# Optimization experiments

Measured on AMD Instinct MI355X. Metric: run time of the kernel, lower is better.

The kernel has to match this reference:

```python
import jax, jax.numpy as jnp
import numpy as np

D_MODEL = 512
NHEAD = 8
MAX_REL = 256  # max_relative_position


def _linear(x, w, b):
    # torch nn.Linear: y = x @ W^T + b, W: [out, in]
    return jnp.einsum('...i,oi->...o', x, w) + b


def setup_inputs() -> dict:
    key = jax.random.key(0)
    ks = jax.random.split(key, 16)
    B, S, D = 32, 512, D_MODEL
    s = 0.02
    inp = {
        'query': jax.random.normal(ks[0], (B, S, D), jnp.float32),
        'key':   jax.random.normal(ks[1], (B, S, D), jnp.float32),
        'value': jax.random.normal(ks[2], (B, S, D), jnp.float32),
        # local attention projections (torch Linear weights [out,in])
        'wq': jax.random.normal(ks[3], (D, D), jnp.float32) * s,
        'bq': jnp.zeros((D,), jnp.float32),
        'wk': jax.random.normal(ks[4], (D, D), jnp.float32) * s,
        'bk': jnp.zeros((D,), jnp.float32),
        'wv': jax.random.normal(ks[5], (D, D), jnp.float32) * s,
        'bv': jnp.zeros((D,), jnp.float32),
        'wo': jax.random.normal(ks[6], (D, D), jnp.float32) * s,
        'bo': jnp.zeros((D,), jnp.float32),
        # relative-position key embedding table [2*MAX_REL+1, head_dim]
        'rel_k': jax.random.normal(ks[7], (2 * MAX_REL + 1, D // NHEAD), jnp.float32) * s,
        # global nn.MultiheadAttention (nhead//2 heads): packed in_proj + out_proj
        'g_in_w': jax.random.normal(ks[8], (3 * D, D), jnp.float32) * s,
        'g_in_b': jnp.zeros((3 * D,), jnp.float32),
        'g_out_w': jax.random.normal(ks[9], (D, D), jnp.float32) * s,
        'g_out_b': jnp.zeros((D,), jnp.float32),
    }
    return inp


def reference(query, key, value, wq, bq, wk, bk, wv, bv, wo, bo, rel_k,
              g_in_w, g_in_b, g_out_w, g_out_b):
    B, S, D = query.shape
    H, hd = NHEAD, D // NHEAD

    # --- local attention with relative-position bias ---
    q = _linear(query, wq, bq).reshape(B, S, H, hd).transpose(0, 2, 1, 3)  # [B,H,S,hd]
    k = _linear(key,   wk, bk).reshape(B, S, H, hd).transpose(0, 2, 1, 3)
    v = _linear(value, wv, bv).reshape(B, S, H, hd).transpose(0, 2, 1, 3)

    scores = jnp.einsum('bhqd,bhkd->bhqk', q, k) / jnp.sqrt(jnp.float32(hd))

    # relative positions: distance[i,j] = j - i, clamped, shifted to [0, 2*MAX_REL]
    idx = jnp.arange(S)
    rel_ids = jnp.clip(idx[None, :] - idx[:, None], -MAX_REL, MAX_REL) + MAX_REL  # [S,S]
    rel_pos_k = rel_k[rel_ids]  # [S, S, hd]
    scores = scores + jnp.einsum('bhld,lrd->bhlr', q, rel_pos_k)

    attn = jax.nn.softmax(scores, axis=-1)
    local = jnp.einsum('bhqk,bhkd->bhqd', attn, v)
    local = local.transpose(0, 2, 1, 3).reshape(B, S, D)

    # --- global MHA with H//2 heads ---
    Hg = H // 2
    hdg = D // Hg
    qg = _linear(query, g_in_w[:D], g_in_b[:D]).reshape(B, S, Hg, hdg).transpose(0, 2, 1, 3)
    kg = _linear(key,   g_in_w[D:2 * D], g_in_b[D:2 * D]).reshape(B, S, Hg, hdg).transpose(0, 2, 1, 3)
    vg = _linear(value, g_in_w[2 * D:], g_in_b[2 * D:]).reshape(B, S, Hg, hdg).transpose(0, 2, 1, 3)
    gs = jnp.einsum('bhqd,bhkd->bhqk', qg, kg) / jnp.sqrt(jnp.float32(hdg))
    ga = jax.nn.softmax(gs, axis=-1)
    g = jnp.einsum('bhqk,bhkd->bhqd', ga, vg).transpose(0, 2, 1, 3).reshape(B, S, D)
    g = _linear(g, g_out_w, g_out_b)

    combined = 0.7 * local + 0.3 * g
    return _linear(combined, wo, bo)
```

## Files before the change

kernel.cpp:

```cpp
#include <hip/hip_runtime.h>

typedef __attribute__((ext_vector_type(8))) short bh8;
typedef __attribute__((ext_vector_type(4))) float f4;

#define DEVI static __device__ __forceinline__

DEVI unsigned short f2b(float f) {
  union { float f; unsigned u; } v; v.f = f;
  unsigned r = v.u + 0x7fffu + ((v.u >> 16) & 1u);
  return (unsigned short)(r >> 16);
}
DEVI float b2f(unsigned short h) {
  union { unsigned u; float f; } v; v.u = ((unsigned)h) << 16;
  return v.f;
}
DEVI f4 mfma16(bh8 a, bh8 b, f4 c) {
  return __builtin_amdgcn_mfma_f32_16x16x32_bf16(a, b, c, 0, 0, 0);
}
DEVI void gload_lds16(const unsigned short* g, unsigned short* l) {
  __builtin_amdgcn_global_load_lds(
      (const __attribute__((address_space(1))) void*)(g),
      (__attribute__((address_space(3))) void*)(l), 16, 0, 0);
}

__global__ __launch_bounds__(256) void prep_x_kern(
    const float* __restrict__ q, const float* __restrict__ k, const float* __restrict__ v,
    unsigned short* __restrict__ xq, unsigned short* __restrict__ xk, unsigned short* __restrict__ xv) {
  long i = ((long)blockIdx.x * 256 + threadIdx.x) * 4;
  if (i >= 8388608L) return;
  float4 a = *(const float4*)(q + i);
  float4 b = *(const float4*)(k + i);
  float4 c = *(const float4*)(v + i);
  union { unsigned short s[4]; uint2 u; } pa, pb, pc;
  pa.s[0] = f2b(a.x); pa.s[1] = f2b(a.y); pa.s[2] = f2b(a.z); pa.s[3] = f2b(a.w);
  pb.s[0] = f2b(b.x); pb.s[1] = f2b(b.y); pb.s[2] = f2b(b.z); pb.s[3] = f2b(b.w);
  pc.s[0] = f2b(c.x); pc.s[1] = f2b(c.y); pc.s[2] = f2b(c.z); pc.s[3] = f2b(c.w);
  *(uint2*)(xq + i) = pa.u;
  *(uint2*)(xk + i) = pb.u;
  *(uint2*)(xv + i) = pc.u;
}

__global__ __launch_bounds__(256) void prep_w_kern(
    const float* __restrict__ wq, const float* __restrict__ wk, const float* __restrict__ wv,
    const float* __restrict__ g_in_w, const float* __restrict__ g_out_w,
    const float* __restrict__ wo, const float* __restrict__ rel_k,
    const float* __restrict__ bgo, const float* __restrict__ bo,
    unsigned short* __restrict__ Wq, unsigned short* __restrict__ Wk, unsigned short* __restrict__ Wv,
    unsigned short* __restrict__ Wo_, unsigned short* __restrict__ WgoT,
    unsigned short* __restrict__ Bfin, unsigned short* __restrict__ Rk,
    float* __restrict__ bias2) {
  if (blockIdx.x >= 2337) {
    int o = (blockIdx.x - 2337) * 256 + threadIdx.x;
    if (o < 512) {
      const float* r = wo + (long)o * 512;
      float s = 0.f;
#pragma unroll 4
      for (int m = 0; m < 512; m += 4) {
        float4 a = *(const float4*)(r + m);
        float4 b = *(const float4*)(bgo + m);
        s += a.x * b.x + a.y * b.y + a.z * b.z + a.w * b.w;
      }
      bias2[o] = bo[o] + 0.3f * s;
    }
    return;
  }
  long i = ((long)blockIdx.x * 256 + threadIdx.x) * 4;
  if (i >= 2392128L) return;
  if (i >= 2097152L && i < 2359296L) {
    long off = i - 2097152L;
    int ii = (int)(off >> 9), p = (int)(off & 511);
    union { unsigned short s[4]; uint2 u; } w;
#pragma unroll
    for (int tt = 0; tt < 4; tt++) w.s[tt] = f2b(g_out_w[(p + tt) * 512 + ii]);
    *(uint2*)(WgoT + off) = w.u;
    return;
  }
  const float* src; unsigned short* dst; long off; float sc = 1.0f;
  if (i < 524288L)        { dst = Wq;  off = i; src = (i < 262144L) ? wq + i : g_in_w + (i - 262144L); }
  else if (i < 1048576L)  { long j = i - 524288L;  dst = Wk;  off = j; src = (j < 262144L) ? wk + j : g_in_w + j; }
  else if (i < 1572864L)  { long j = i - 1048576L; dst = Wv;  off = j; src = (j < 262144L) ? wv + j : g_in_w + 262144L + j; }
  else if (i < 1835008L)  { long j = i - 1572864L; dst = Wo_; off = j; src = wo + j; }
  else if (i < 2097152L)  { long j = i - 1835008L; int col = (int)(j >> 9), k = (int)(j & 511);
                            dst = Bfin; off = (long)col * 1024 + k; src = wo + j; sc = 0.7f; }
  else                    { long j = i - 2359296L; dst = Rk;  off = j; src = rel_k + j; }
  float4 f = *(const float4*)src;
  union { unsigned short s[4]; uint2 u; } p;
  p.s[0] = f2b(f.x * sc); p.s[1] = f2b(f.y * sc); p.s[2] = f2b(f.z * sc); p.s[3] = f2b(f.w * sc);
  *(uint2*)(dst + off) = p.u;
}

__global__ __launch_bounds__(256) void gemm3_kern(
    const unsigned short* __restrict__ Xq, const unsigned short* __restrict__ Xk,
    const unsigned short* __restrict__ Xv,
    const unsigned short* __restrict__ Wq, const unsigned short* __restrict__ Wk,
    const unsigned short* __restrict__ Wv,
    const float* __restrict__ bq, const float* __restrict__ bk, const float* __restrict__ bv,
    const float* __restrict__ g_in_b,
    unsigned short* __restrict__ Yq, unsigned short* __restrict__ Yk_,
    unsigned short* __restrict__ Yvt_l, unsigned short* __restrict__ Yvt_g,
    const unsigned short* __restrict__ Wo_, const unsigned short* __restrict__ WgoT,
    unsigned short* __restrict__ Bfin) {
  __shared__ unsigned short lsA[128 * 32];
  __shared__ unsigned short lsB[128 * 32];
  const int t = threadIdx.x;
  const int lane = t & 63, w = t >> 6;
  const int l15 = lane & 15, g = lane >> 4, g4 = g * 4;
  const int gs8 = (g ^ ((l15 >> 1) & 3)) * 8;
  const int n = blockIdx.x;

  const unsigned short *Ap, *Bp;
  const float *b0 = nullptr, *b1 = nullptr;
  int seg, rb, cb;
  if (n < 3072) {
    seg = n >> 10;
    int m = n & 1023;
    int x = m >> 3, c = m & 7;
    rb = (c * 16 + (x & 15)) * 128;
    cb = (x >> 4) * 128;
    Ap = (seg == 0) ? Xq : (seg == 1) ? Xk : Xv;
    Bp = (seg == 0) ? Wq : (seg == 1) ? Wk : Wv;
    b0 = (seg == 0) ? bq : (seg == 1) ? bk : bv;
    b1 = g_in_b + seg * 512;
  } else {
    seg = 3;
    int m2 = n - 3072;
    rb = (m2 & 3) * 128; cb = (m2 >> 2) * 128;
    Ap = Wo_; Bp = WgoT;
  }

  const int wr = (w >> 1) * 64, wc = (w & 1) * 64;
  const int r0 = t >> 2, r1 = 64 + (t >> 2);
  const int k0i = ((t & 3) ^ ((t >> 3) & 3)) * 8;

  const unsigned short* pa0 = Ap + (long)(rb + r0) * 512 + k0i;
  const unsigned short* pa1 = Ap + (long)(rb + r1) * 512 + k0i;
  const unsigned short* pb0 = Bp + (long)(cb + r0) * 512 + k0i;
  const unsigned short* pb1 = Bp + (long)(cb + r1) * 512 + k0i;
  unsigned short* dA0 = lsA + w * 512;
  unsigned short* dA1 = lsA + 2048 + w * 512;
  unsigned short* dB0 = lsB + w * 512;
  unsigned short* dB1 = lsB + 2048 + w * 512;

  f4 acc[4][4] = {};
  for (int k0 = 0; k0 < 512; k0 += 32) {
    __syncthreads();
    gload_lds16(pa0 + k0, dA0);
    gload_lds16(pa1 + k0, dA1);
    gload_lds16(pb0 + k0, dB0);
    gload_lds16(pb1 + k0, dB1);
    __syncthreads();
    bh8 af[4], bf[4];
#pragma unroll
    for (int m = 0; m < 4; m++) af[m] = *(const bh8*)(lsA + (wr + m * 16 + l15) * 32 + gs8);
#pragma unroll
    for (int nn = 0; nn < 4; nn++) bf[nn] = *(const bh8*)(lsB + (wc + nn * 16 + l15) * 32 + gs8);
    __builtin_amdgcn_s_setprio(1);
#pragma unroll
    for (int m = 0; m < 4; m++)
#pragma unroll
      for (int nn = 0; nn < 4; nn++)
        acc[m][nn] = mfma16(af[m], bf[nn], acc[m][nn]);
    __builtin_amdgcn_s_setprio(0);
  }

  if (seg == 3) {
#pragma unroll
// ... 28 lines not shown
        if (col < 512) {
          int hh = col >> 6, d = col & 63;
          *(uint2*)(Yvt_l + (((long)(bb * 8 + hh) * 64 + d) << 9) + s) = make_uint2(lo, hi);
        } else {
          int c2 = col - 512, hg = c2 >> 7, dg = c2 & 127;
          *(uint2*)(Yvt_g + (((long)(bb * 4 + hg) * 128 + dg) << 9) + s) = make_uint2(lo, hi);
        }
      }
    return;
  }
  unsigned short* Yo = (seg == 0) ? Yq : Yk_;
#pragma unroll
  for (int m = 0; m < 4; m++)
#pragma unroll
    for (int nn = 0; nn < 4; nn++)
#pragma unroll
      for (int j = 0; j < 4; j++) {
        int row = rb + wr + m * 16 + g4 + j;
        int col = cb + wc + nn * 16 + l15;
        float v = acc[m][nn][j] + ((col < 512) ? b0[col] : b1[col - 512]);
        Yo[(long)row * 1024 + col] = f2b(v);
      }
}

__global__ __launch_bounds__(256) void gemm_fin_kern(
    const unsigned short* __restrict__ A, const unsigned short* __restrict__ Bw,
    const float* __restrict__ bias0, float* __restrict__ outf) {
  __shared__ unsigned short lsA[128 * 32];
  __shared__ unsigned short lsB[128 * 32];
  const int t = threadIdx.x;
  const int lane = t & 63, w = t >> 6;
  const int l15 = lane & 15, g = lane >> 4, g4 = g * 4;
  const int gs8 = (g ^ ((l15 >> 1) & 3)) * 8;
  int n = blockIdx.x;
  int x = n >> 3, c = n & 7;
  const int rb = (c * 16 + (x & 15)) * 128;
  const int cb = (x >> 4) * 128;
  const int wr = (w >> 1) * 64, wc = (w & 1) * 64;
  const int r0 = t >> 2, r1 = 64 + (t >> 2);
  const int k0i = ((t & 3) ^ ((t >> 3) & 3)) * 8;

  const unsigned short* pa0 = A + (long)(rb + r0) * 1024 + k0i;
  const unsigned short* pa1 = A + (long)(rb + r1) * 1024 + k0i;
  const unsigned short* pb0 = Bw + (long)(cb + r0) * 1024 + k0i;
  const unsigned short* pb1 = Bw + (long)(cb + r1) * 1024 + k0i;
  unsigned short* dA0 = lsA + w * 512;
  unsigned short* dA1 = lsA + 2048 + w * 512;
  unsigned short* dB0 = lsB + w * 512;
  unsigned short* dB1 = lsB + 2048 + w * 512;

  f4 acc[4][4] = {};
  for (int k0 = 0; k0 < 1024; k0 += 32) {
    __syncthreads();
    gload_lds16(pa0 + k0, dA0);
    gload_lds16(pa1 + k0, dA1);
    gload_lds16(pb0 + k0, dB0);
    gload_lds16(pb1 + k0, dB1);
    __syncthreads();
    bh8 af[4], bf[4];
#pragma unroll
    for (int m = 0; m < 4; m++) af[m] = *(const bh8*)(lsA + (wr + m * 16 + l15) * 32 + gs8);
#pragma unroll
    for (int nn = 0; nn < 4; nn++) bf[nn] = *(const bh8*)(lsB + (wc + nn * 16 + l15) * 32 + gs8);
    __builtin_amdgcn_s_setprio(1);
#pragma unroll
    for (int m = 0; m < 4; m++)
#pragma unroll
      for (int nn = 0; nn < 4; nn++)
        acc[m][nn] = mfma16(af[m], bf[nn], acc[m][nn]);
    __builtin_amdgcn_s_setprio(0);
  }
#pragma unroll
  for (int m = 0; m < 4; m++)
#pragma unroll
    for (int nn = 0; nn < 4; nn++)
#pragma unroll
      for (int j = 0; j < 4; j++) {
        int row = rb + wr + m * 16 + g4 + j;
        int col = cb + wc + nn * 16 + l15;
        outf[(long)row * 512 + col] = acc[m][nn][j] + bias0[col];
      }
}

__global__ __launch_bounds__(512, 4) void attn_local_kern(
    const unsigned short* __restrict__ Yq, const unsigned short* __restrict__ Yk,
    const unsigned short* __restrict__ Yvt, const unsigned short* __restrict__ relk,
    unsigned short* __restrict__ outC) {
  __shared__ unsigned short kv[2][8192];
  __shared__ unsigned short buf[32 * 524];
  __shared__ float redbuf[8][32];

  const int t = threadIdx.x, lane = t & 63, w = t >> 6;
  const int l15 = lane & 15, g = lane >> 4, g8 = g * 8;
  int n = blockIdx.x;
  int bid = (n & 7) * 512 + (n >> 3);
  const int qt = bid & 15;
  const int h = (bid >> 4) & 7;
  const int b = bid >> 7;
  const int qb = qt * 32;
  const long base = ((long)(b * 512)) * 1024 + h * 64;
  const long vbase = ((long)(b * 8 + h)) * 64 * 512;

#define STAGE_K(ROFF, BUF) { \
    const int c_ = t & 7; \
    _Pragma("unroll") \
    for (int it = 0; it < 2; it++) { \
      int rr = it * 64 + (t >> 3); \
      gload_lds16(Yk + base + (long)((ROFF) + rr) * 1024 + ((c_ ^ (rr & 7)) * 8), \
                  kv[BUF] + it * 4096 + w * 512); \
    } }
#define STAGE_V(COFF, BUF) { \
    const int c_ = t & 15; \
    _Pragma("unroll") \
    for (int it = 0; it < 2; it++) { \
      int dd_ = it * 32 + (t >> 4); \
      gload_lds16(Yvt + vbase + (long)dd_ * 512 + (COFF) + ((c_ ^ (dd_ & 15)) * 8), \
                  kv[BUF] + it * 4096 + w * 512); \
    } }
#define QK(CH) { \
    int rl = w * 16 + l15; \
    const unsigned short* kb_ = kv[(CH) & 1]; \
    bh8 k0 = *(const bh8*)(kb_ + rl * 64 + ((g ^ (rl & 7)) * 8)); \
    bh8 k1 = *(const bh8*)(kb_ + rl * 64 + (((g + 4) ^ (rl & 7)) * 8)); \
    _Pragma("unroll") \
    for (int mm = 0; mm < 2; mm++) { \
      f4 a = {}; \
      a = mfma16(qf[mm][0], k0, a); \
      a = mfma16(qf[mm][1], k1, a); \
      sc[mm][CH] = a; \
    } }
#define GATHER(CH) { \
    _Pragma("unroll") \
    for (int mm = 0; mm < 2; mm++) \
    _Pragma("unroll") \
    for (int j = 0; j < 4; j++) { \
      int lr = mm * 16 + g * 4 + j; \
      int rowb = lr * 524; \
      int idx = rowb + 256 - (qb + lr) + (CH) * 128 + w * 16 + l15; \
      idx = idx < rowb ? rowb : idx; \
      idx = idx > rowb + 512 ? rowb + 512 : idx; \
      float p = exp2f(fmaf(sc[mm][CH][j], 0.18033688011112042f, b2f(buf[idx]))); \
      sc[mm][CH][j] = p; \
      rs[mm][j] += p; \
    } }

  STAGE_K(0, 0);

  bh8 qf[2][2];
#pragma unroll
  for (int mm = 0; mm < 2; mm++) {
    const unsigned short* qp = Yq + base + (long)(qb + mm * 16 + l15) * 1024 + g8;
    qf[mm][0] = *(const bh8*)(qp);
    qf[mm][1] = *(const bh8*)(qp + 32);
  }

  for (int tt = w; tt < 33; tt += 8) {
    int ri = tt * 16 + l15; if (ri > 512) ri = 512;
    const unsigned short* rp = relk + ri * 64 + g8;
    bh8 rf0 = *(const bh8*)(rp), rf1 = *(const bh8*)(rp + 32);
    int col = tt * 16 + l15;
#pragma unroll
    for (int mm = 0; mm < 2; mm++) {
      f4 a = {};
      a = mfma16(qf[mm][0], rf0, a);
      a = mfma16(qf[mm][1], rf1, a);
      if (col < 524) {
#pragma unroll
        for (int j = 0; j < 4; j++)
          buf[(mm * 16 + g * 4 + j) * 524 + col] = f2b(a[j] * 1.4426950408889634f);
      }
    }
  }
  __syncthreads();

  f4 sc[2][4];
  float rs[2][4] = {};

#pragma unroll
  for (int c = 0; c < 4; c++) {
    if (c < 3) { STAGE_K((c + 1) * 128, (c + 1) & 1); }
    else       { STAGE_V(0, 0); }
    __builtin_amdgcn_s_setprio(1);
    QK(c);
    __builtin_amdgcn_s_setprio(0);
    GATHER(c);
    __syncthreads();
  }

#pragma unroll
  for (int mm = 0; mm < 2; mm++)
#pragma unroll
    for (int j = 0; j < 4; j++) {
      int lr = mm * 16 + g * 4 + j;
      float s = rs[mm][j];
      for (int d = 1; d < 16; d <<= 1) s += __shfl_xor(s, d, 64);
      if (l15 == 0) redbuf[w][lr] = s;
    }
#pragma unroll
  for (int mm = 0; mm < 2; mm++)
#pragma unroll
    for (int ch = 0; ch < 4; ch++) {
      int col = ch * 128 + w * 16 + l15;
#pragma unroll
      for (int j = 0; j < 4; j++)
        buf[(mm * 16 + g * 4 + j) * 524 + col] = f2b(sc[mm][ch][j]);
    }
  __syncthreads();

  const int mmw = w >> 2, dt = w & 3;
  const int dd = dt * 16 + l15;
  float rinvj[4];
#pragma unroll
  for (int j = 0; j < 4; j++) {
    int lr = mmw * 16 + g * 4 + j;
    float s = 0.f;
#pragma unroll
    for (int ww = 0; ww < 8; ww++) s += redbuf[ww][lr];
    rinvj[j] = __builtin_amdgcn_rcpf(s);
  }

  f4 accO = {};
#pragma unroll
  for (int d = 0; d < 4; d++) {
    if (d < 3) { STAGE_V((d + 1) * 128, (d + 1) & 1); }
    const unsigned short* vb_ = kv[d & 1];
    __builtin_amdgcn_s_setprio(1);
#pragma unroll
    for (int ks2 = 0; ks2 < 4; ks2++) {
      union { uint2 u[2]; bh8 v; } pa;
      const unsigned short* pp = buf + (mmw * 16 + l15) * 524 + (d * 4 + ks2) * 32 + g8;
      pa.u[0] = *(const uint2*)(pp);
      pa.u[1] = *(const uint2*)(pp + 4);
      bh8 vv = *(const bh8*)(vb_ + dd * 128 + (((ks2 * 4 + g) ^ (dd & 15)) * 8));
      accO = mfma16(pa.v, vv, accO);
    }
    __builtin_amdgcn_s_setprio(0);
    if (d < 3) __syncthreads();
  }
#pragma unroll
  for (int j = 0; j < 4; j++) {
    int row = qb + mmw * 16 + g * 4 + j;
    outC[((long)(b * 512 + row)) * 1024 + h * 64 + dt * 16 + l15] = f2b(accO[j] * rinvj[j]);
  }
#undef STAGE_K
#undef STAGE_V
#undef QK
#undef GATHER
}

__global__ __launch_bounds__(512) void attn_glob_kern(
    const unsigned short* __restrict__ Yq, const unsigned short* __restrict__ Yk,
    const unsigned short* __restrict__ Yvt, unsigned short* __restrict__ outC) {
  __shared__ unsigned short buf[32 * 520];
  __shared__ float redbuf[8][32];

  const int t = threadIdx.x, lane = t & 63, w = t >> 6;
  const int l15 = lane & 15, g = lane >> 4, g8 = g * 8;
  int n = blockIdx.x;
  int bid = (n & 7) * 256 + (n >> 3);
  const int qt = bid & 15;
  const int hg = (bid >> 4) & 3;
  const int b = bid >> 6;
  const int qb = qt * 32;
  const long base = ((long)(b * 512)) * 1024 + 512 + hg * 128;

  bh8 qf[2][4];
#pragma unroll
  for (int mm = 0; mm < 2; mm++) {
    const unsigned short* qp = Yq + base + (long)(qb + mm * 16 + l15) * 1024 + g8;
#pragma unroll
    for (int ks = 0; ks < 4; ks++) qf[mm][ks] = *(const bh8*)(qp + ks * 32);
  }

  f4 sc[2][4];
  __builtin_amdgcn_s_setprio(1);
#pragma unroll
  for (int ct = 0; ct < 4; ct++) {
    int r = w * 64 + ct * 16 + l15;
    const unsigned short* kp = Yk + base + (long)r * 1024 + g8;
    bh8 kf[4];
#pragma unroll
    for (int ks = 0; ks < 4; ks++) kf[ks] = *(const bh8*)(kp + ks * 32);
#pragma unroll
    for (int mm = 0; mm < 2; mm++) {
      f4 a = {};
#pragma unroll
      for (int ks = 0; ks < 4; ks++) a = mfma16(qf[mm][ks], kf[ks], a);
      sc[mm][ct] = a;
    }
  }
  __builtin_amdgcn_s_setprio(0);

#pragma unroll
  for (int mm = 0; mm < 2; mm++) {
#pragma unroll
    for (int j = 0; j < 4; j++) {
      int lr = mm * 16 + g * 4 + j;
      float s = 0.f;
#pragma unroll
      for (int ct = 0; ct < 4; ct++) {
        float p = exp2f(sc[mm][ct][j] * 0.12751745334f);
        sc[mm][ct][j] = p;
        s += p;
      }
      for (int d = 1; d < 16; d <<= 1) s += __shfl_xor(s, d, 64);
      if (l15 == 0) redbuf[w][lr] = s;
    }
  }
#pragma unroll
  for (int mm = 0; mm < 2; mm++)
#pragma unroll
    for (int ct = 0; ct < 4; ct++) {
      int col = w * 64 + ct * 16 + l15;
#pragma unroll
      for (int j = 0; j < 4; j++)
        buf[(mm * 16 + g * 4 + j) * 520 + col] = f2b(sc[mm][ct][j]);
    }
  __syncthreads();

  float rinv[2][4];
#pragma unroll
  for (int mm = 0; mm < 2; mm++)
#pragma unroll
    for (int j = 0; j < 4; j++) {
      int lr = mm * 16 + g * 4 + j;
      float s = 0.f;
#pragma unroll
      for (int ww = 0; ww < 8; ww++) s += redbuf[ww][lr];
      rinv[mm][j] = __builtin_amdgcn_rcpf(s);
    }

  f4 accO[2] = {};
  const unsigned short* vr = Yvt + ((long)(b * 4 + hg) * 128 + w * 16 + l15) * 512;
  __builtin_amdgcn_s_setprio(1);
#pragma unroll
  for (int ks = 0; ks < 16; ks++) {
    bh8 vb = *(const bh8*)(vr + ks * 32 + g8);
#pragma unroll
    for (int mm = 0; mm < 2; mm++) {
      union { uint2 u[2]; bh8 v; } pa;
      const unsigned short* pp = buf + (mm * 16 + l15) * 520 + ks * 32 + g8;
      pa.u[0] = *(const uint2*)(pp);
      pa.u[1] = *(const uint2*)(pp + 4);
      accO[mm] = mfma16(pa.v, vb, accO[mm]);
    }
  }
  __builtin_amdgcn_s_setprio(0);
#pragma unroll
  for (int mm = 0; mm < 2; mm++)
#pragma unroll
    for (int j = 0; j < 4; j++) {
      int row = qb + mm * 16 + g * 4 + j;
      outC[((long)(b * 512 + row)) * 1024 + 512 + hg * 128 + w * 16 + l15] = f2b(accO[mm][j] * rinv[mm][j]);
    }
}

extern "C" void kernel_launch(void* const* d_in, const int* in_sizes, int n_in,
                              void* d_out, int out_size, void* d_ws, size_t ws_size,
                              hipStream_t stream) {
  const float* query = (const float*)d_in[0];
  const float* key   = (const float*)d_in[1];
  const float* value = (const float*)d_in[2];
  const float* wq = (const float*)d_in[3];   const float* bq = (const float*)d_in[4];
  const float* wk = (const float*)d_in[5];   const float* bk = (const float*)d_in[6];
  const float* wv = (const float*)d_in[7];   const float* bv = (const float*)d_in[8];
  const float* wo = (const float*)d_in[9];   const float* bo = (const float*)d_in[10];
  const float* rel_k = (const float*)d_in[11];
  const float* g_in_w = (const float*)d_in[12];  const float* g_in_b = (const float*)d_in[13];
  const float* g_out_w = (const float*)d_in[14]; const float* g_out_b = (const float*)d_in[15];

  unsigned short* p = (unsigned short*)d_ws;
  unsigned short* Xq = p;            p += 8388608;
  unsigned short* Xk = p;            p += 8388608;
  unsigned short* Xv = p;            p += 8388608;
  unsigned short* Yq = p;            p += 16777216;
  unsigned short* Yk = p;            p += 16777216;
  unsigned short* Yvt_l = p;         p += 8388608;
  unsigned short* Yvt_g = p;         p += 8388608;
  unsigned short* Wq = p;            p += 524288;
  unsigned short* Wk = p;            p += 524288;
  unsigned short* Wv = p;            p += 524288;
  unsigned short* Wo_ = p;           p += 262144;
  unsigned short* WgoT = p;          p += 262144;
  unsigned short* Bfin = p;          p += 524288;
  unsigned short* Rk = p;            p += 32832;
  float* bias2 = (float*)p;          p += 1024;
  unsigned short* CAT = Xq;

  prep_x_kern<<<8192, 256, 0, stream>>>(query, key, value, Xq, Xk, Xv);
  prep_w_kern<<<2339, 256, 0, stream>>>(wq, wk, wv, g_in_w, g_out_w, wo, rel_k,
                                        g_out_b, bo,
                                        Wq, Wk, Wv, Wo_, WgoT, Bfin, Rk, bias2);

  gemm3_kern<<<3088, 256, 0, stream>>>(Xq, Xk, Xv, Wq, Wk, Wv, bq, bk, bv, g_in_b,
                                       Yq, Yk, Yvt_l, Yvt_g, Wo_, WgoT, Bfin);

  attn_local_kern<<<4096, 512, 0, stream>>>(Yq, Yk, Yvt_l, Rk, CAT);
  attn_glob_kern<<<2048, 512, 0, stream>>>(Yq, Yk, Yvt_g, CAT);

  gemm_fin_kern<<<512, 256, 0, stream>>>(CAT, Bfin, bias2, (float*)d_out);
}
```

Baseline: 342.4 us.

## Merge prep kernels and interleave local/global attention into one launch

Combines the activation and weight conversion kernels into a single launch. It also fuses the local and global attention kernels into one grid, interleaving two local blocks per global block so both kinds run concurrently. The intent is to remove launch overhead and the tail and idle gaps between dependent-free kernels. In exchange, the global path now shares the local path's register bounds and its larger shared-memory allocation, which may reduce its occupancy.

After: 341.2 us. Within noise of the previous version (-0.3%).

```diff
diff --git a/kernel.cpp b/kernel.cpp
--- a/kernel.cpp
+++ b/kernel.cpp
@@ -23,34 +23,34 @@
       (__attribute__((address_space(3))) void*)(l), 16, 0, 0);
 }
 
-__global__ __launch_bounds__(256) void prep_x_kern(
+__global__ __launch_bounds__(256) void prep_all_kern(
     const float* __restrict__ q, const float* __restrict__ k, const float* __restrict__ v,
-    unsigned short* __restrict__ xq, unsigned short* __restrict__ xk, unsigned short* __restrict__ xv) {
-  long i = ((long)blockIdx.x * 256 + threadIdx.x) * 4;
-  if (i >= 8388608L) return;
-  float4 a = *(const float4*)(q + i);
-  float4 b = *(const float4*)(k + i);
-  float4 c = *(const float4*)(v + i);
-  union { unsigned short s[4]; uint2 u; } pa, pb, pc;
-  pa.s[0] = f2b(a.x); pa.s[1] = f2b(a.y); pa.s[2] = f2b(a.z); pa.s[3] = f2b(a.w);
-  pb.s[0] = f2b(b.x); pb.s[1] = f2b(b.y); pb.s[2] = f2b(b.z); pb.s[3] = f2b(b.w);
-  pc.s[0] = f2b(c.x); pc.s[1] = f2b(c.y); pc.s[2] = f2b(c.z); pc.s[3] = f2b(c.w);
-  *(uint2*)(xq + i) = pa.u;
-  *(uint2*)(xk + i) = pb.u;
-  *(uint2*)(xv + i) = pc.u;
-}
-
-__global__ __launch_bounds__(256) void prep_w_kern(
     const float* __restrict__ wq, const float* __restrict__ wk, const float* __restrict__ wv,
     const float* __restrict__ g_in_w, const float* __restrict__ g_out_w,
     const float* __restrict__ wo, const float* __restrict__ rel_k,
     const float* __restrict__ bgo, const float* __restrict__ bo,
+    unsigned short* __restrict__ xq, unsigned short* __restrict__ xk, unsigned short* __restrict__ xv,
     unsigned short* __restrict__ Wq, unsigned short* __restrict__ Wk, unsigned short* __restrict__ Wv,
     unsigned short* __restrict__ Wo_, unsigned short* __restrict__ WgoT,
     unsigned short* __restrict__ Bfin, unsigned short* __restrict__ Rk,
     float* __restrict__ bias2) {
-  if (blockIdx.x >= 2337) {
-    int o = (blockIdx.x - 2337) * 256 + threadIdx.x;
+  if (blockIdx.x < 8192) {
+    long i = ((long)blockIdx.x * 256 + threadIdx.x) * 4;
+    float4 a = *(const float4*)(q + i);
+    float4 b = *(const float4*)(k + i);
+    float4 c = *(const float4*)(v + i);
+    union { unsigned short s[4]; uint2 u; } pa, pb, pc;
+    pa.s[0] = f2b(a.x); pa.s[1] = f2b(a.y); pa.s[2] = f2b(a.z); pa.s[3] = f2b(a.w);
+    pb.s[0] = f2b(b.x); pb.s[1] = f2b(b.y); pb.s[2] = f2b(b.z); pb.s[3] = f2b(b.w);
+    pc.s[0] = f2b(c.x); pc.s[1] = f2b(c.y); pc.s[2] = f2b(c.z); pc.s[3] = f2b(c.w);
+    *(uint2*)(xq + i) = pa.u;
+    *(uint2*)(xk + i) = pb.u;
+    *(uint2*)(xv + i) = pc.u;
+    return;
+  }
+  int bw = blockIdx.x - 8192;
+  if (bw >= 2337) {
+    int o = (bw - 2337) * 256 + threadIdx.x;
     if (o < 512) {
       const float* r = wo + (long)o * 512;
       float s = 0.f;
@@ -64,7 +64,7 @@
     }
     return;
   }
-  long i = ((long)blockIdx.x * 256 + threadIdx.x) * 4;
+  long i = ((long)bw * 256 + threadIdx.x) * 4;
   if (i >= 2392128L) return;
   if (i >= 2097152L && i < 2359296L) {
     long off = i - 2097152L;
@@ -80,8 +80,8 @@
   else if (i < 1048576L)  { long j = i - 524288L;  dst = Wk;  off = j; src = (j < 262144L) ? wk + j : g_in_w + j; }
   else if (i < 1572864L)  { long j = i - 1048576L; dst = Wv;  off = j; src = (j < 262144L) ? wv + j : g_in_w + 262144L + j; }
   else if (i < 1835008L)  { long j = i - 1572864L; dst = Wo_; off = j; src = wo + j; }
-  else if (i < 2097152L)  { long j = i - 1835008L; int col = (int)(j >> 9), k = (int)(j & 511);
-                            dst = Bfin; off = (long)col * 1024 + k; src = wo + j; sc = 0.7f; }
+  else if (i < 2097152L)  { long j = i - 1835008L; int col = (int)(j >> 9), kk = (int)(j & 511);
+                            dst = Bfin; off = (long)col * 1024 + kk; src = wo + j; sc = 0.7f; }
   else                    { long j = i - 2359296L; dst = Rk;  off = j; src = rel_k + j; }
   float4 f = *(const float4*)src;
   union { unsigned short s[4]; uint2 u; } p;
@@ -276,24 +276,28 @@
       }
 }
 
-__global__ __launch_bounds__(512, 4) void attn_local_kern(
+__global__ __launch_bounds__(512, 4) void attn_kern(
     const unsigned short* __restrict__ Yq, const unsigned short* __restrict__ Yk,
-    const unsigned short* __restrict__ Yvt, const unsigned short* __restrict__ relk,
-    unsigned short* __restrict__ outC) {
+    const unsigned short* __restrict__ Yvt_l, const unsigned short* __restrict__ Yvt_g,
+    const unsigned short* __restrict__ relk, unsigned short* __restrict__ outC) {
   __shared__ unsigned short kv[2][8192];
   __shared__ unsigned short buf[32 * 524];
   __shared__ float redbuf[8][32];
 
   const int t = threadIdx.x, lane = t & 63, w = t >> 6;
   const int l15 = lane & 15, g = lane >> 4, g8 = g * 8;
-  int n = blockIdx.x;
-  int bid = (n & 7) * 512 + (n >> 3);
-  const int qt = bid & 15;
-  const int h = (bid >> 4) & 7;
-  const int b = bid >> 7;
-  const int qb = qt * 32;
-  const long base = ((long)(b * 512)) * 1024 + h * 64;
-  const long vbase = ((long)(b * 8 + h)) * 64 * 512;
+  const int n = blockIdx.x;
+  const int grp = n / 3, r3 = n - grp * 3;
+
+  if (r3 < 2) {
+    int ln = grp * 2 + r3;
+    int bid = (ln & 7) * 512 + (ln >> 3);
+    const int qt = bid & 15;
+    const int h = (bid >> 4) & 7;
+    const int b = bid >> 7;
+    const int qb = qt * 32;
+    const long base = ((long)(b * 512)) * 1024 + h * 64;
+    const long vbase = ((long)(b * 8 + h)) * 64 * 512;
 
 #define STAGE_K(ROFF, BUF) { \
     const int c_ = t & 7; \
@@ -308,7 +312,7 @@
     _Pragma("unroll") \
     for (int it = 0; it < 2; it++) { \
       int dd_ = it * 32 + (t >> 4); \
-      gload_lds16(Yvt + vbase + (long)dd_ * 512 + (COFF) + ((c_ ^ (dd_ & 15)) * 8), \
+      gload_lds16(Yvt_l + vbase + (long)dd_ * 512 + (COFF) + ((c_ ^ (dd_ & 15)) * 8), \
                   kv[BUF] + it * 4096 + w * 512); \
     } }
 #define QK(CH) { \
@@ -338,215 +342,207 @@
       rs[mm][j] += p; \
     } }
 
-  STAGE_K(0, 0);
-
-  bh8 qf[2][2];
-#pragma unroll
-  for (int mm = 0; mm < 2; mm++) {
-    const unsigned short* qp = Yq + base + (long)(qb + mm * 16 + l15) * 1024 + g8;
-    qf[mm][0] = *(const bh8*)(qp);
-    qf[mm][1] = *(const bh8*)(qp + 32);
-  }
-
-  for (int tt = w; tt < 33; tt += 8) {
-    int ri = tt * 16 + l15; if (ri > 512) ri = 512;
-    const unsigned short* rp = relk + ri * 64 + g8;
-    bh8 rf0 = *(const bh8*)(rp), rf1 = *(const bh8*)(rp + 32);
-    int col = tt * 16 + l15;
+    STAGE_K(0, 0);
+
+    bh8 qf[2][2];
 #pragma unroll
     for (int mm = 0; mm < 2; mm++) {
-      f4 a = {};
-      a = mfma16(qf[mm][0], rf0, a);
-      a = mfma16(qf[mm][1], rf1, a);
-      if (col < 524) {
+      const unsigned short* qp = Yq + base + (long)(qb + mm * 16 + l15) * 1024 + g8;
+      qf[mm][0] = *(const bh8*)(qp);
+      qf[mm][1] = *(const bh8*)(qp + 32);
+    }
+
+    for (int tt = w; tt < 33; tt += 8) {
+      int ri = tt * 16 + l15; if (ri > 512) ri = 512;
+      const unsigned short* rp = relk + ri * 64 + g8;
+      bh8 rf0 = *(const bh8*)(rp), rf1 = *(const bh8*)(rp + 32);
+      int col = tt * 16 + l15;
+#pragma unroll
+      for (int mm = 0; mm < 2; mm++) {
+        f4 a = {};
+        a = mfma16(qf[mm][0], rf0, a);
+        a = mfma16(qf[mm][1], rf1, a);
+        if (col < 524) {
+#pragma unroll
+          for (int j = 0; j < 4; j++)
+            buf[(mm * 16 + g * 4 + j) * 524 + col] = f2b(a[j] * 1.4426950408889634f);
+        }
+      }
+    }
+    __syncthreads();
+
+    f4 sc[2][4];
+    float rs[2][4] = {};
+
+#pragma unroll
+    for (int c = 0; c < 4; c++) {
+      if (c < 3) { STAGE_K((c + 1) * 128, (c + 1) & 1); }
+      else       { STAGE_V(0, 0); }
+      __builtin_amdgcn_s_setprio(1);
+      QK(c);
+      __builtin_amdgcn_s_setprio(0);
+      GATHER(c);
+      __syncthreads();
+    }
+
+#pragma unroll
+    for (int mm = 0; mm < 2; mm++)
+#pragma unroll
+      for (int j = 0; j < 4; j++) {
+        int lr = mm * 16 + g * 4 + j;
+        float s = rs[mm][j];
+        for (int d = 1; d < 16; d <<= 1) s += __shfl_xor(s, d, 64);
+        if (l15 == 0) redbuf[w][lr] = s;
+      }
+#pragma unroll
+    for (int mm = 0; mm < 2; mm++)
+#pragma unroll
+      for (int ch = 0; ch < 4; ch++) {
+        int col = ch * 128 + w * 16 + l15;
 #pragma unroll
         for (int j = 0; j < 4; j++)
-          buf[(mm * 16 + g * 4 + j) * 524 + col] = f2b(a[j] * 1.4426950408889634f);
-      }
-    }
-  }
-  __syncthreads();
-
-  f4 sc[2][4];
-  float rs[2][4] = {};
-
-#pragma unroll
-  for (int c = 0; c < 4; c++) {
-    if (c < 3) { STAGE_K((c + 1) * 128, (c + 1) & 1); }
-    else       { STAGE_V(0, 0); }
-    __builtin_amdgcn_s_setprio(1);
-    QK(c);
-    __builtin_amdgcn_s_setprio(0);
-    GATHER(c);
-    __syncthreads();
-  }
-
-#pragma unroll
-  for (int mm = 0; mm < 2; mm++)
+          buf[(mm * 16 + g * 4 + j) * 524 + col] = f2b(sc[mm][ch][j]);
+      }
+    __syncthreads();
+
+    const int mmw = w >> 2, dt = w & 3;
+    const int dd = dt * 16 + l15;
+    float rinvj[4];
 #pragma unroll
     for (int j = 0; j < 4; j++) {
-      int lr = mm * 16 + g * 4 + j;
-      float s = rs[mm][j];
-      for (int d = 1; d < 16; d <<= 1) s += __shfl_xor(s, d, 64);
-      if (l15 == 0) redbuf[w][lr] = s;
-    }
-#pragma unroll
-  for (int mm = 0; mm < 2; mm++)
-#pragma unroll
-    for (int ch = 0; ch < 4; ch++) {
-      int col = ch * 128 + w * 16 + l15;
-#pragma unroll
-      for (int j = 0; j < 4; j++)
-        buf[(mm * 16 + g * 4 + j) * 524 + col] = f2b(sc[mm][ch][j]);
-    }
-  __syncthreads();
-
-  const int mmw = w >> 2, dt = w & 3;
-  const int dd = dt * 16 + l15;
-  float rinvj[4];
-#pragma unroll
-  for (int j = 0; j < 4; j++) {
-    int lr = mmw * 16 + g * 4 + j;
-    float s = 0.f;
-#pragma unroll
-    for (int ww = 0; ww < 8; ww++) s += redbuf[ww][lr];
-    rinvj[j] = __builtin_amdgcn_rcpf(s);
-  }
-
-  f4 accO = {};
-#pragma unroll
-  for (int d = 0; d < 4; d++) {
-    if (d < 3) { STAGE_V((d + 1) * 128, (d + 1) & 1); }
-    const unsigned short* vb_ = kv[d & 1];
-    __builtin_amdgcn_s_setprio(1);
-#pragma unroll
-    for (int ks2 = 0; ks2 < 4; ks2++) {
-      union { uint2 u[2]; bh8 v; } pa;
-      const unsigned short* pp = buf + (mmw * 16 + l15) * 524 + (d * 4 + ks2) * 32 + g8;
-      pa.u[0] = *(const uint2*)(pp);
-      pa.u[1] = *(const uint2*)(pp + 4);
-      bh8 vv = *(const bh8*)(vb_ + dd * 128 + (((ks2 * 4 + g) ^ (dd & 15)) * 8));
-      accO = mfma16(pa.v, vv, accO);
-    }
-    __builtin_amdgcn_s_setprio(0);
-    if (d < 3) __syncthreads();
-  }
-#pragma unroll
-  for (int j = 0; j < 4; j++) {
-    int row = qb + mmw * 16 + g * 4 + j;
-    outC[((long)(b * 512 + row)) * 1024 + h * 64 + dt * 16 + l15] = f2b(accO[j] * rinvj[j]);
-  }
+      int lr = mmw * 16 + g * 4 + j;
+      float s = 0.f;
+#pragma unroll
+      for (int ww = 0; ww < 8; ww++) s += redbuf[ww][lr];
+      rinvj[j] = __builtin_amdgcn_rcpf(s);
+    }
+
+    f4 accO = {};
+#pragma unroll
+    for (int d = 0; d < 4; d++) {
+      if (d < 3) { STAGE_V((d + 1) * 128, (d + 1) & 1); }
+      const unsigned short* vb_ = kv[d & 1];
+      __builtin_amdgcn_s_setprio(1);
+#pragma unroll
+      for (int ks2 = 0; ks2 < 4; ks2++) {
+        union { uint2 u[2]; bh8 v; } pa;
+        const unsigned short* pp = buf + (mmw * 16 + l15) * 524 + (d * 4 + ks2) * 32 + g8;
+        pa.u[0] = *(const uint2*)(pp);
+        pa.u[1] = *(const uint2*)(pp + 4);
+        bh8 vv = *(const bh8*)(vb_ + dd * 128 + (((ks2 * 4 + g) ^ (dd & 15)) * 8));
+        accO = mfma16(pa.v, vv, accO);
+      }
+      __builtin_amdgcn_s_setprio(0);
+      if (d < 3) __syncthreads();
+    }
+#pragma unroll
+    for (int j = 0; j < 4; j++) {
+      int row = qb + mmw * 16 + g * 4 + j;
+      outC[((long)(b * 512 + row)) * 1024 + h * 64 + dt * 16 + l15] = f2b(accO[j] * rinvj[j]);
+    }
 #undef STAGE_K
 #undef STAGE_V
 #undef QK
 #undef GATHER
-}
-
-__global__ __launch_bounds__(512) void attn_glob_kern(
-    const unsigned short* __restrict__ Yq, const unsigned short* __restrict__ Yk,
-    const unsigned short* __restrict__ Yvt, unsigned short* __restrict__ outC) {
-  __shared__ unsigned short buf[32 * 520];
-  __shared__ float redbuf[8][32];
-
-  const int t = threadIdx.x, lane = t & 63, w = t >> 6;
-  const int l15 = lane & 15, g = lane >> 4, g8 = g * 8;
-  int n = blockIdx.x;
-  int bid = (n & 7) * 256 + (n >> 3);
-  const int qt = bid & 15;
-  const int hg = (bid >> 4) & 3;
-  const int b = bid >> 6;
-  const int qb = qt * 32;
-  const long base = ((long)(b * 512)) * 1024 + 512 + hg * 128;
-
-  bh8 qf[2][4];
-#pragma unroll
-  for (int mm = 0; mm < 2; mm++) {
-    const unsigned short* qp = Yq + base + (long)(qb + mm * 16 + l15) * 1024 + g8;
-#pragma unroll
-    for (int ks = 0; ks < 4; ks++) qf[mm][ks] = *(const bh8*)(qp + ks * 32);
-  }
-
-  f4 sc[2][4];
-  __builtin_amdgcn_s_setprio(1);
-#pragma unroll
-  for (int ct = 0; ct < 4; ct++) {
-    int r = w * 64 + ct * 16 + l15;
-    const unsigned short* kp = Yk + base + (long)r * 1024 + g8;
-    bh8 kf[4];
-#pragma unroll
-    for (int ks = 0; ks < 4; ks++) kf[ks] = *(const bh8*)(kp + ks * 32);
+  } else {
+    int gn = grp;
+    int bid = (gn & 7) * 256 + (gn >> 3);
+    const int qt = bid & 15;
+    const int hg = (bid >> 4) & 3;
+    const int b = bid >> 6;
+    const int qb = qt * 32;
+    const long base = ((long)(b * 512)) * 1024 + 512 + hg * 128;
+
+    bh8 qf[2][4];
 #pragma unroll
     for (int mm = 0; mm < 2; mm++) {
-      f4 a = {};
-#pragma unroll
-      for (int ks = 0; ks < 4; ks++) a = mfma16(qf[mm][ks], kf[ks], a);
-      sc[mm][ct] = a;
-    }
-  }
-  __builtin_amdgcn_s_setprio(0);
-
-#pragma unroll
-  for (int mm = 0; mm < 2; mm++) {
-#pragma unroll
-    for (int j = 0; j < 4; j++) {
-      int lr = mm * 16 + g * 4 + j;
-      float s = 0.f;
+      const unsigned short* qp = Yq + base + (long)(qb + mm * 16 + l15) * 1024 + g8;
+#pragma unroll
+      for (int ks = 0; ks < 4; ks++) qf[mm][ks] = *(const bh8*)(qp + ks * 32);
+    }
+
+    f4 sc[2][4];
+    __builtin_amdgcn_s_setprio(1);
+#pragma unroll
+    for (int ct = 0; ct < 4; ct++) {
+      int r = w * 64 + ct * 16 + l15;
+      const unsigned short* kp = Yk + base + (long)r * 1024 + g8;
+      bh8 kf[4];
+#pragma unroll
+      for (int ks = 0; ks < 4; ks++) kf[ks] = *(const bh8*)(kp + ks * 32);
+#pragma unroll
+      for (int mm = 0; mm < 2; mm++) {
+        f4 a = {};
+#pragma unroll
+        for (int ks = 0; ks < 4; ks++) a = mfma16(qf[mm][ks], kf[ks], a);
+        sc[mm][ct] = a;
+      }
+    }
+    __builtin_amdgcn_s_setprio(0);
+
+#pragma unroll
+    for (int mm = 0; mm < 2; mm++) {
+#pragma unroll
+      for (int j = 0; j < 4; j++) {
+        int lr = mm * 16 + g * 4 + j;
+        float s = 0.f;
+#pragma unroll
+        for (int ct = 0; ct < 4; ct++) {
+          float p = exp2f(sc[mm][ct][j] * 0.12751745334f);
+          sc[mm][ct][j] = p;
+          s += p;
+        }
+        for (int d = 1; d < 16; d <<= 1) s += __shfl_xor(s, d, 64);
+        if (l15 == 0) redbuf[w][lr] = s;
+      }
+    }
+#pragma unroll
+    for (int mm = 0; mm < 2; mm++)
 #pragma unroll
       for (int ct = 0; ct < 4; ct++) {
-        float p = exp2f(sc[mm][ct][j] * 0.12751745334f);
-        sc[mm][ct][j] = p;
-        s += p;
-      }
-      for (int d = 1; d < 16; d <<= 1) s += __shfl_xor(s, d, 64);
-      if (l15 == 0) redbuf[w][lr] = s;
-    }
-  }
-#pragma unroll
-  for (int mm = 0; mm < 2; mm++)
-#pragma unroll
-    for (int ct = 0; ct < 4; ct++) {
-      int col = w * 64 + ct * 16 + l15;
-#pragma unroll
-      for (int j = 0; j < 4; j++)
-        buf[(mm * 16 + g * 4 + j) * 520 + col] = f2b(sc[mm][ct][j]);
-    }
-  __syncthreads();
-
-  float rinv[2][4];
-#pragma unroll
-  for (int mm = 0; mm < 2; mm++)
-#pragma unroll
-    for (int j = 0; j < 4; j++) {
-      int lr = mm * 16 + g * 4 + j;
-      float s = 0.f;
-#pragma unroll
-      for (int ww = 0; ww < 8; ww++) s += redbuf[ww][lr];
-      rinv[mm][j] = __builtin_amdgcn_rcpf(s);
-    }
-
-  f4 accO[2] = {};
-  const unsigned short* vr = Yvt + ((long)(b * 4 + hg) * 128 + w * 16 + l15) * 512;
-  __builtin_amdgcn_s_setprio(1);
-#pragma unroll
-  for (int ks = 0; ks < 16; ks++) {
-    bh8 vb = *(const bh8*)(vr + ks * 32 + g8);
-#pragma unroll
-    for (int mm = 0; mm < 2; mm++) {
-      union { uint2 u[2]; bh8 v; } pa;
-      const unsigned short* pp = buf + (mm * 16 + l15) * 520 + ks * 32 + g8;
-      pa.u[0] = *(const uint2*)(pp);
-      pa.u[1] = *(const uint2*)(pp + 4);
-      accO[mm] = mfma16(pa.v, vb, accO[mm]);
-    }
-  }
-  __builtin_amdgcn_s_setprio(0);
-#pragma unroll
-  for (int mm = 0; mm < 2; mm++)
-#pragma unroll
-    for (int j = 0; j < 4; j++) {
-      int row = qb + mm * 16 + g * 4 + j;
-      outC[((long)(b * 512 + row)) * 1024 + 512 + hg * 128 + w * 16 + l15] = f2b(accO[mm][j] * rinv[mm][j]);
-    }
+        int col = w * 64 + ct * 16 + l15;
+#pragma unroll
+        for (int j = 0; j < 4; j++)
+          buf[(mm * 16 + g * 4 + j) * 524 + col] = f2b(sc[mm][ct][j]);
+      }
+    __syncthreads();
+
+    float rinv[2][4];
+#pragma unroll
+    for (int mm = 0; mm < 2; mm++)
+#pragma unroll
+      for (int j = 0; j < 4; j++) {
+        int lr = mm * 16 + g * 4 + j;
+        float s = 0.f;
+#pragma unroll
+        for (int ww = 0; ww < 8; ww++) s += redbuf[ww][lr];
+        rinv[mm][j] = __builtin_amdgcn_rcpf(s);
+      }
+
+    f4 accO[2] = {};
+    const unsigned short* vr = Yvt_g + ((long)(b * 4 + hg) * 128 + w * 16 + l15) * 512;
+    __builtin_amdgcn_s_setprio(1);
+#pragma unroll
+    for (int ks = 0; ks < 16; ks++) {
+      bh8 vb = *(const bh8*)(vr + ks * 32 + g8);
+#pragma unroll
+      for (int mm = 0; mm < 2; mm++) {
+        union { uint2 u[2]; bh8 v; } pa;
+        const unsigned short* pp = buf + (mm * 16 + l15) * 524 + ks * 32 + g8;
+        pa.u[0] = *(const uint2*)(pp);
+        pa.u[1] = *(const uint2*)(pp + 4);
+        accO[mm] = mfma16(pa.v, vb, accO[mm]);
+      }
+    }
+    __builtin_amdgcn_s_setprio(0);
+#pragma unroll
+    for (int mm = 0; mm < 2; mm++)
+#pragma unroll
+      for (int j = 0; j < 4; j++) {
+        int row = qb + mm * 16 + g * 4 + j;
+        outC[((long)(b * 512 + row)) * 1024 + 512 + hg * 128 + w * 16 + l15] = f2b(accO[mm][j] * rinv[mm][j]);
+      }
+  }
 }
 
 extern "C" void kernel_launch(void* const* d_in, const int* in_sizes, int n_in,
@@ -581,16 +577,15 @@
   float* bias2 = (float*)p;          p += 1024;
   unsigned short* CAT = Xq;
 
-  prep_x_kern<<<8192, 256, 0, stream>>>(query, key, value, Xq, Xk, Xv);
-  prep_w_kern<<<2339, 256, 0, stream>>>(wq, wk, wv, g_in_w, g_out_w, wo, rel_k,
-                                        g_out_b, bo,
-                                        Wq, Wk, Wv, Wo_, WgoT, Bfin, Rk, bias2);
+  prep_all_kern<<<10531, 256, 0, stream>>>(query, key, value,
+                                           wq, wk, wv, g_in_w, g_out_w, wo, rel_k,
+                                           g_out_b, bo,
+                                           Xq, Xk, Xv, Wq, Wk, Wv, Wo_, WgoT, Bfin, Rk, bias2);
 
   gemm3_kern<<<3088, 256, 0, stream>>>(Xq, Xk, Xv, Wq, Wk, Wv, bq, bk, bv, g_in_b,
                                        Yq, Yk, Yvt_l, Yvt_g, Wo_, WgoT, Bfin);
 
-  attn_local_kern<<<4096, 512, 0, stream>>>(Yq, Yk, Yvt_l, Rk, CAT);
-  attn_glob_kern<<<2048, 512, 0, stream>>>(Yq, Yk, Yvt_g, CAT);
+  attn_kern<<<6144, 512, 0, stream>>>(Yq, Yk, Yvt_l, Yvt_g, Rk, CAT);
 
   gemm_fin_kern<<<512, 256, 0, stream>>>(CAT, Bfin, bias2, (float*)d_out);
 }
```

## Stage global-attention K/V through double-buffered LDS and merge prep kernels

Applied to the files above, without the earlier changes.

The global attention kernel no longer has each wave read K and V straight from global memory. K and V tiles are now staged into a double-buffered, XOR-swizzled LDS buffer with global_load_lds, so the next tile loads while MFMAs run on the current one. The work is split so each wave handles a 16-row query slice against a 16-column key slice per chunk, and launch bounds request 4 blocks per CU. The two prep kernels are also merged into one launch to save launch overhead. In exchange the kernel uses more LDS and adds many more block-wide barriers, which may limit occupancy.

After: 313.4 us. -8.5%, faster.

```diff
diff --git a/kernel.cpp b/kernel.cpp
--- a/kernel.cpp
+++ b/kernel.cpp
@@ -23,34 +23,34 @@
       (__attribute__((address_space(3))) void*)(l), 16, 0, 0);
 }
 
-__global__ __launch_bounds__(256) void prep_x_kern(
+__global__ __launch_bounds__(256) void prep_all_kern(
     const float* __restrict__ q, const float* __restrict__ k, const float* __restrict__ v,
-    unsigned short* __restrict__ xq, unsigned short* __restrict__ xk, unsigned short* __restrict__ xv) {
-  long i = ((long)blockIdx.x * 256 + threadIdx.x) * 4;
-  if (i >= 8388608L) return;
-  float4 a = *(const float4*)(q + i);
-  float4 b = *(const float4*)(k + i);
-  float4 c = *(const float4*)(v + i);
-  union { unsigned short s[4]; uint2 u; } pa, pb, pc;
-  pa.s[0] = f2b(a.x); pa.s[1] = f2b(a.y); pa.s[2] = f2b(a.z); pa.s[3] = f2b(a.w);
-  pb.s[0] = f2b(b.x); pb.s[1] = f2b(b.y); pb.s[2] = f2b(b.z); pb.s[3] = f2b(b.w);
-  pc.s[0] = f2b(c.x); pc.s[1] = f2b(c.y); pc.s[2] = f2b(c.z); pc.s[3] = f2b(c.w);
-  *(uint2*)(xq + i) = pa.u;
-  *(uint2*)(xk + i) = pb.u;
-  *(uint2*)(xv + i) = pc.u;
-}
-
-__global__ __launch_bounds__(256) void prep_w_kern(
     const float* __restrict__ wq, const float* __restrict__ wk, const float* __restrict__ wv,
     const float* __restrict__ g_in_w, const float* __restrict__ g_out_w,
     const float* __restrict__ wo, const float* __restrict__ rel_k,
     const float* __restrict__ bgo, const float* __restrict__ bo,
+    unsigned short* __restrict__ xq, unsigned short* __restrict__ xk, unsigned short* __restrict__ xv,
     unsigned short* __restrict__ Wq, unsigned short* __restrict__ Wk, unsigned short* __restrict__ Wv,
     unsigned short* __restrict__ Wo_, unsigned short* __restrict__ WgoT,
     unsigned short* __restrict__ Bfin, unsigned short* __restrict__ Rk,
     float* __restrict__ bias2) {
-  if (blockIdx.x >= 2337) {
-    int o = (blockIdx.x - 2337) * 256 + threadIdx.x;
+  if (blockIdx.x < 8192) {
+    long i = ((long)blockIdx.x * 256 + threadIdx.x) * 4;
+    float4 a = *(const float4*)(q + i);
+    float4 b = *(const float4*)(k + i);
+    float4 c = *(const float4*)(v + i);
+    union { unsigned short s[4]; uint2 u; } pa, pb, pc;
+    pa.s[0] = f2b(a.x); pa.s[1] = f2b(a.y); pa.s[2] = f2b(a.z); pa.s[3] = f2b(a.w);
+    pb.s[0] = f2b(b.x); pb.s[1] = f2b(b.y); pb.s[2] = f2b(b.z); pb.s[3] = f2b(b.w);
+    pc.s[0] = f2b(c.x); pc.s[1] = f2b(c.y); pc.s[2] = f2b(c.z); pc.s[3] = f2b(c.w);
+    *(uint2*)(xq + i) = pa.u;
+    *(uint2*)(xk + i) = pb.u;
+    *(uint2*)(xv + i) = pc.u;
+    return;
+  }
+  int bw = blockIdx.x - 8192;
+  if (bw >= 2337) {
+    int o = (bw - 2337) * 256 + threadIdx.x;
     if (o < 512) {
       const float* r = wo + (long)o * 512;
       float s = 0.f;
@@ -64,7 +64,7 @@
     }
     return;
   }
-  long i = ((long)blockIdx.x * 256 + threadIdx.x) * 4;
+  long i = ((long)bw * 256 + threadIdx.x) * 4;
   if (i >= 2392128L) return;
   if (i >= 2097152L && i < 2359296L) {
     long off = i - 2097152L;
@@ -80,8 +80,8 @@
   else if (i < 1048576L)  { long j = i - 524288L;  dst = Wk;  off = j; src = (j < 262144L) ? wk + j : g_in_w + j; }
   else if (i < 1572864L)  { long j = i - 1048576L; dst = Wv;  off = j; src = (j < 262144L) ? wv + j : g_in_w + 262144L + j; }
   else if (i < 1835008L)  { long j = i - 1572864L; dst = Wo_; off = j; src = wo + j; }
-  else if (i < 2097152L)  { long j = i - 1835008L; int col = (int)(j >> 9), k = (int)(j & 511);
-                            dst = Bfin; off = (long)col * 1024 + k; src = wo + j; sc = 0.7f; }
+  else if (i < 2097152L)  { long j = i - 1835008L; int col = (int)(j >> 9), kk = (int)(j & 511);
+                            dst = Bfin; off = (long)col * 1024 + kk; src = wo + j; sc = 0.7f; }
   else                    { long j = i - 2359296L; dst = Rk;  off = j; src = rel_k + j; }
   float4 f = *(const float4*)src;
   union { unsigned short s[4]; uint2 u; } p;
@@ -442,9 +442,10 @@
 #undef GATHER
 }
 
-__global__ __launch_bounds__(512) void attn_glob_kern(
+__global__ __launch_bounds__(512, 4) void attn_glob_kern(
     const unsigned short* __restrict__ Yq, const unsigned short* __restrict__ Yk,
     const unsigned short* __restrict__ Yvt, unsigned short* __restrict__ outC) {
+  __shared__ unsigned short kv[2][8192];
   __shared__ unsigned short buf[32 * 520];
   __shared__ float redbuf[8][32];
 
@@ -457,89 +458,112 @@
   const int b = bid >> 6;
   const int qb = qt * 32;
   const long base = ((long)(b * 512)) * 1024 + 512 + hg * 128;
-
-  bh8 qf[2][4];
-#pragma unroll
-  for (int mm = 0; mm < 2; mm++) {
-    const unsigned short* qp = Yq + base + (long)(qb + mm * 16 + l15) * 1024 + g8;
-#pragma unroll
-    for (int ks = 0; ks < 4; ks++) qf[mm][ks] = *(const bh8*)(qp + ks * 32);
-  }
-
-  f4 sc[2][4];
-  __builtin_amdgcn_s_setprio(1);
-#pragma unroll
-  for (int ct = 0; ct < 4; ct++) {
-    int r = w * 64 + ct * 16 + l15;
-    const unsigned short* kp = Yk + base + (long)r * 1024 + g8;
-    bh8 kf[4];
-#pragma unroll
-    for (int ks = 0; ks < 4; ks++) kf[ks] = *(const bh8*)(kp + ks * 32);
-#pragma unroll
-    for (int mm = 0; mm < 2; mm++) {
-      f4 a = {};
-#pragma unroll
-      for (int ks = 0; ks < 4; ks++) a = mfma16(qf[mm][ks], kf[ks], a);
-      sc[mm][ct] = a;
-    }
-  }
-  __builtin_amdgcn_s_setprio(0);
-
-#pragma unroll
-  for (int mm = 0; mm < 2; mm++) {
+  const long vgbase = ((long)(b * 4 + hg)) * 128 * 512;
+
+#define STAGE_GK(KC, BUF) { \
+    const int c_ = t & 15; \
+    _Pragma("unroll") \
+    for (int it = 0; it < 2; it++) { \
+      int rr = it * 32 + (t >> 4); \
+      gload_lds16(Yk + base + (long)((KC) * 64 + rr) * 1024 + ((c_ ^ (rr & 15)) * 8), \
+                  kv[BUF] + it * 4096 + w * 512); \
+    } }
+#define STAGE_GV(KC, BUF) { \
+    const int c_ = t & 7; \
+    _Pragma("unroll") \
+    for (int it = 0; it < 2; it++) { \
+      int dd_ = it * 64 + (t >> 3); \
+      gload_lds16(Yvt + vgbase + (long)dd_ * 512 + (KC) * 64 + ((c_ ^ (dd_ & 7)) * 8), \
+                  kv[BUF] + it * 4096 + w * 512); \
+    } }
+
+  const int mmq = w >> 2, wq4 = w & 3;
+
+  STAGE_GK(0, 0);
+
+  bh8 qf[4];
+  {
+    const unsigned short* qp = Yq + base + (long)(qb + mmq * 16 + l15) * 1024 + g8;
+#pragma unroll
+    for (int ks = 0; ks < 4; ks++) qf[ks] = *(const bh8*)(qp + ks * 32);
+  }
+  __syncthreads();
+
+  f4 sc8[8];
+#pragma unroll
+  for (int kc = 0; kc < 8; kc++) {
+    if (kc < 7) { STAGE_GK(kc + 1, (kc + 1) & 1); }
+    else        { STAGE_GV(0, 0); }
+    const unsigned short* kb_ = kv[kc & 1];
+    const int rl = wq4 * 16 + l15;
+    __builtin_amdgcn_s_setprio(1);
+    f4 a = {};
+#pragma unroll
+    for (int ks = 0; ks < 4; ks++) {
+      bh8 kf = *(const bh8*)(kb_ + rl * 128 + (((ks * 4 + g) ^ (rl & 15)) * 8));
+      a = mfma16(qf[ks], kf, a);
+    }
+    sc8[kc] = a;
+    __builtin_amdgcn_s_setprio(0);
+    __syncthreads();
+  }
+
+#pragma unroll
+  for (int j = 0; j < 4; j++) {
+    int lr = mmq * 16 + g * 4 + j;
+    float s = 0.f;
+#pragma unroll
+    for (int kc = 0; kc < 8; kc++) {
+      float p = exp2f(sc8[kc][j] * 0.12751745334f);
+      sc8[kc][j] = p;
+      s += p;
+    }
+    for (int d = 1; d < 16; d <<= 1) s += __shfl_xor(s, d, 64);
+    if (l15 == 0) redbuf[w][lr] = s;
+  }
+  __syncthreads();
+
+#pragma unroll
+  for (int kc = 0; kc < 8; kc++) {
+    int col = kc * 64 + wq4 * 16 + l15;
+#pragma unroll
+    for (int j = 0; j < 4; j++)
+      buf[(mmq * 16 + g * 4 + j) * 520 + col] = f2b(sc8[kc][j]);
+  }
+  float rinv[2][4];
+#pragma unroll
+  for (int mm = 0; mm < 2; mm++)
 #pragma unroll
     for (int j = 0; j < 4; j++) {
       int lr = mm * 16 + g * 4 + j;
-      float s = 0.f;
-#pragma unroll
-      for (int ct = 0; ct < 4; ct++) {
-        float p = exp2f(sc[mm][ct][j] * 0.12751745334f);
-        sc[mm][ct][j] = p;
-        s += p;
+      float s = redbuf[mm * 4 + 0][lr] + redbuf[mm * 4 + 1][lr] +
+                redbuf[mm * 4 + 2][lr] + redbuf[mm * 4 + 3][lr];
+      rinv[mm][j] = __builtin_amdgcn_rcpf(s);
+    }
+  __syncthreads();
+
+  const int dd = w * 16 + l15;
+  f4 accO[2] = {};
+#pragma unroll
+  for (int kc = 0; kc < 8; kc++) {
+    if (kc < 7) { STAGE_GV(kc + 1, (kc + 1) & 1); }
+    const unsigned short* vb_ = kv[kc & 1];
+    __builtin_amdgcn_s_setprio(1);
+#pragma unroll
+    for (int ks2 = 0; ks2 < 2; ks2++) {
+      bh8 vv = *(const bh8*)(vb_ + dd * 64 + (((ks2 * 4 + g) ^ (dd & 7)) * 8));
+#pragma unroll
+      for (int mm = 0; mm < 2; mm++) {
+        union { uint2 u[2]; bh8 v; } pa;
+        const unsigned short* pp = buf + (mm * 16 + l15) * 520 + kc * 64 + ks2 * 32 + g8;
+        pa.u[0] = *(const uint2*)(pp);
+        pa.u[1] = *(const uint2*)(pp + 4);
+        accO[mm] = mfma16(pa.v, vv, accO[mm]);
       }
-      for (int d = 1; d < 16; d <<= 1) s += __shfl_xor(s, d, 64);
-      if (l15 == 0) redbuf[w][lr] = s;
-    }
-  }
-#pragma unroll
-  for (int mm = 0; mm < 2; mm++)
-#pragma unroll
-    for (int ct = 0; ct < 4; ct++) {
-      int col = w * 64 + ct * 16 + l15;
-#pragma unroll
-      for (int j = 0; j < 4; j++)
-        buf[(mm * 16 + g * 4 + j) * 520 + col] = f2b(sc[mm][ct][j]);
-    }
-  __syncthreads();
-
-  float rinv[2][4];
-#pragma unroll
-  for (int mm = 0; mm < 2; mm++)
-#pragma unroll
-    for (int j = 0; j < 4; j++) {
-      int lr = mm * 16 + g * 4 + j;
-      float s = 0.f;
-#pragma unroll
-      for (int ww = 0; ww < 8; ww++) s += redbuf[ww][lr];
-      rinv[mm][j] = __builtin_amdgcn_rcpf(s);
-    }
-
-  f4 accO[2] = {};
-  const unsigned short* vr = Yvt + ((long)(b * 4 + hg) * 128 + w * 16 + l15) * 512;
-  __builtin_amdgcn_s_setprio(1);
-#pragma unroll
-  for (int ks = 0; ks < 16; ks++) {
-    bh8 vb = *(const bh8*)(vr + ks * 32 + g8);
-#pragma unroll
-    for (int mm = 0; mm < 2; mm++) {
-      union { uint2 u[2]; bh8 v; } pa;
-      const unsigned short* pp = buf + (mm * 16 + l15) * 520 + ks * 32 + g8;
-      pa.u[0] = *(const uint2*)(pp);
-      pa.u[1] = *(const uint2*)(pp + 4);
-      accO[mm] = mfma16(pa.v, vb, accO[mm]);
-    }
-  }
-  __builtin_amdgcn_s_setprio(0);
+    }
+    __builtin_amdgcn_s_setprio(0);
+    if (kc < 7) __syncthreads();
+  }
 #pragma unroll
   for (int mm = 0; mm < 2; mm++)
 #pragma unroll
@@ -547,6 +571,8 @@
       int row = qb + mm * 16 + g * 4 + j;
       outC[((long)(b * 512 + row)) * 1024 + 512 + hg * 128 + w * 16 + l15] = f2b(accO[mm][j] * rinv[mm][j]);
     }
+#undef STAGE_GK
+#undef STAGE_GV
 }
 
 extern "C" void kernel_launch(void* const* d_in, const int* in_sizes, int n_in,
@@ -581,10 +607,10 @@
   float* bias2 = (float*)p;          p += 1024;
   unsigned short* CAT = Xq;
 
-  prep_x_kern<<<8192, 256, 0, stream>>>(query, key, value, Xq, Xk, Xv);
-  prep_w_kern<<<2339, 256, 0, stream>>>(wq, wk, wv, g_in_w, g_out_w, wo, rel_k,
-                                        g_out_b, bo,
-                                        Wq, Wk, Wv, Wo_, WgoT, Bfin, Rk, bias2);
+  prep_all_kern<<<10531, 256, 0, stream>>>(query, key, value,
+                                           wq, wk, wv, g_in_w, g_out_w, wo, rel_k,
+                                           g_out_b, bo,
+                                           Xq, Xk, Xv, Wq, Wk, Wv, Wo_, WgoT, Bfin, Rk, bias2);
 
   gemm3_kern<<<3088, 256, 0, stream>>>(Xq, Xk, Xv, Wq, Wk, Wv, bq, bk, bv, g_in_b,
                                        Yq, Yk, Yvt_l, Yvt_g, Wo_, WgoT, Bfin);
```
